# Optimization experiments

Hardware: AMD Instinct MI355X
Metric: run time of the kernel (lower is better)

## Reference

```python
import jax, jax.numpy as jnp
import numpy as np

B, N, D = 2, 2048, 2048
H = 16
HD = D // H  # 128


def setup_inputs() -> dict:
    key = jax.random.key(0)
    k1, k2, k3 = jax.random.split(key, 3)
    x = jax.random.normal(k1, (B, N, D), dtype=jnp.float32)
    # Linear weights stored as [in, out] so y = x @ W matches torch's x @ W.T
    Wq = jax.random.normal(k2, (D, D), dtype=jnp.float32) * (D ** -0.5)
    Wo = jax.random.normal(k3, (D, D), dtype=jnp.float32) * (D ** -0.5)
    bo = jnp.zeros((D,), dtype=jnp.float32)
    return {"x": x, "Wq": Wq, "Wo": Wo, "bo": bo}


def reference(x, Wq, Wo, bo):
    # NOTE: source module (faithfully) projects q, k, v all with q_matrix.
    b, n, d = x.shape
    q = x @ Wq                                   # [B, N, D]
    qh = q.reshape(b, n, H, HD).transpose(0, 2, 1, 3)  # [B, H, N, HD]
    scores = jnp.einsum("bhnd,bhmd->bhnm", qh, qh) * (HD ** -0.5)  # [B,H,N,N]
    attn = jax.nn.softmax(scores, axis=-1)
    y = jnp.einsum("bhnm,bhmd->bhnd", attn, qh)  # [B, H, N, HD]
    y = y.transpose(0, 2, 1, 3).reshape(b, n, d)  # [B, N, D]
    return y @ Wo + bo
```

## Files before the change

kernel.cpp:

```cpp
#include <hip/hip_runtime.h>
#include <hip/hip_bf16.h>

#define BATCH 2
#define SEQ   2048
#define DIM   2048
#define NHEAD 16
#define HDIM  128

#define KSTRIDE 136
#define VSTRIDE 72
#define PSTRIDE 72

typedef __bf16 bf16;
typedef __attribute__((ext_vector_type(2))) __bf16 bf16x2;
typedef __attribute__((ext_vector_type(4))) __bf16 bf16x4;
typedef __attribute__((ext_vector_type(8))) __bf16 bf16x8;
typedef __attribute__((ext_vector_type(4))) float f32x4;

__device__ __forceinline__ void load_lds16(const bf16* g, bf16* l) {
    __builtin_amdgcn_global_load_lds((const __attribute__((address_space(1))) void*)g,
                                     (__attribute__((address_space(3))) void*)l, 16, 0, 0);
}

__device__ __forceinline__ float exp2_hw(float x) { return __builtin_amdgcn_exp2f(x); }

__global__ __launch_bounds__(256)
void prep_kernel(const float* __restrict__ x, bf16* __restrict__ xb,
                 const float* __restrict__ Wq, bf16* __restrict__ Wtq,
                 const float* __restrict__ Wo, bf16* __restrict__ Wto)
{
    __shared__ bf16 T[64 * 72];
    const int bid = blockIdx.x;
    if (bid < 4096) {
        const size_t i = ((size_t)bid * 256 + threadIdx.x) * 8;
        const float4 f0 = *(const float4*)(x + i);
        const float4 f1 = *(const float4*)(x + i + 4);
        *(bf16x8*)(xb + i) = (bf16x8){(bf16)f0.x, (bf16)f0.y, (bf16)f0.z, (bf16)f0.w,
                                      (bf16)f1.x, (bf16)f1.y, (bf16)f1.z, (bf16)f1.w};
        return;
    }
    int t = bid - 4096;
    const float* W  = (t < 1024) ? Wq : Wo;
    bf16*        Wt = (t < 1024) ? Wtq : Wto;
    t &= 1023;
    const int kb = (t >> 5) * 64, nb = (t & 31) * 64;

    const int a = threadIdx.x & 31;
    const int g = threadIdx.x >> 5;
    {
        const float* s0 = W + (size_t)(kb + 2 * a) * DIM + nb + g * 8;
        const float4 r0a = *(const float4*)(s0);
        const float4 r0b = *(const float4*)(s0 + 4);
        const float4 r1a = *(const float4*)(s0 + DIM);
        const float4 r1b = *(const float4*)(s0 + DIM + 4);
        float v0[8] = {r0a.x, r0a.y, r0a.z, r0a.w, r0b.x, r0b.y, r0b.z, r0b.w};
        float v1[8] = {r1a.x, r1a.y, r1a.z, r1a.w, r1b.x, r1b.y, r1b.z, r1b.w};
        #pragma unroll
        for (int i = 0; i < 8; ++i)
            *(bf16x2*)&T[(g * 8 + i) * 72 + 2 * a] = (bf16x2){(bf16)v0[i], (bf16)v1[i]};
    }
    __syncthreads();

    const int r  = threadIdx.x >> 2;
    const int k0 = (threadIdx.x & 3) * 16;
    bf16x8 o0 = *(const bf16x8*)&T[r * 72 + k0];
    bf16x8 o1 = *(const bf16x8*)&T[r * 72 + k0 + 8];
    *(bf16x8*)(Wt + (size_t)(nb + r) * DIM + kb + k0)     = o0;
    *(bf16x8*)(Wt + (size_t)(nb + r) * DIM + kb + k0 + 8) = o1;
}

#define GEMM_PHASE(S, VM, DO_STAGE)                                            \
    {                                                                          \
        const bf16* Aq = Ls + ((S) & 3) * 12288;                               \
        const bf16* Bq = Aq + 4096;                                            \
        bf16x8 a[4], b[4];                                                     \
        _Pragma("unroll")                                                      \
        for (int i = 0; i < 4; ++i) a[i] = *(const bf16x8*)(Aq + offA[i]);     \
        _Pragma("unroll")                                                      \
        for (int j = 0; j < 4; ++j) b[j] = *(const bf16x8*)(Bq + offB[j]);     \
        if (DO_STAGE) {                                                        \
            bf16* lb = Ls + (((S) + 3) & 3) * 12288 + wave * 512;              \
            const int ko = ((S) + 3) * 32;                                     \
            load_lds16(gA + ko, lb);                                           \
            load_lds16(gB0 + ko, lb + 4096);                                   \
            load_lds16(gB1 + ko, lb + 8192);                                   \
        }                                                                      \
        __builtin_amdgcn_s_barrier();                                          \
        __builtin_amdgcn_s_setprio(1);                                         \
        _Pragma("unroll")                                                      \
        for (int i = 0; i < 4; ++i) {                                          \
            _Pragma("unroll")                                                  \
            for (int j = 0; j < 4; ++j)                                        \
                acc[i][j] = __builtin_amdgcn_mfma_f32_16x16x32_bf16(a[i], b[j], acc[i][j], 0, 0, 0); \
        }                                                                      \
        __builtin_amdgcn_s_setprio(0);                                         \
        if ((VM) == 6)      asm volatile("s_waitcnt vmcnt(6)" ::: "memory");   \
        else if ((VM) == 3) asm volatile("s_waitcnt vmcnt(3)" ::: "memory");   \
        else if ((VM) == 0) asm volatile("s_waitcnt vmcnt(0)" ::: "memory");   \
        if ((VM) >= 0) {                                                       \
            __builtin_amdgcn_s_barrier();                                      \
            asm volatile("" ::: "memory");                                     \
        }                                                                      \
    }

template<bool OUT_F32_BIAS>
__global__ __launch_bounds__(512, 2)
void gemm_bt8(const bf16* __restrict__ A, const bf16* __restrict__ Bt,
              const float* __restrict__ bias, void* __restrict__ Cptr,
              int M, int N, int K)
{
    __shared__ bf16 Ls[4 * 12288];

    const int tid  = threadIdx.x;
    const int wave = tid >> 6;
    const int lane = tid & 63;
    const int quad = lane >> 4;
    const int l16  = lane & 15;
    const int wr   = wave >> 2;
    const int wc   = wave & 3;

    const int cpx = gridDim.x >> 3;
    const int logical = (blockIdx.x & 7) * cpx + (blockIdx.x >> 3);
    const int rowBase = (logical >> 3) * 128;
    const int colBase = (logical & 7) * 256;

    int offA[4], offB[4];
    #pragma unroll
    for (int i = 0; i < 4; ++i) {
        int e = (wr * 64 + i * 16 + l16) * 32 + quad * 8;
        offA[i] = e ^ (((e >> 6) & 3) << 3);
    }
    #pragma unroll
    for (int j = 0; j < 4; ++j) {
        int e = (wc * 64 + j * 16 + l16) * 32 + quad * 8;
        offB[j] = e ^ (((e >> 6) & 3) << 3);
    }

    const int oA  = wave * 512 + lane * 8;
    const int eA  = oA ^ (((oA >> 6) & 3) << 3);
    const bf16* gA  = A  + (size_t)(rowBase + (eA >> 5)) * K + (eA & 31);
    const int oB0 = wave * 512 + lane * 8;
    const int eB0 = oB0 ^ (((oB0 >> 6) & 3) << 3);
    const bf16* gB0 = Bt + (size_t)(colBase + (eB0 >> 5)) * K + (eB0 & 31);
    const int oB1 = 4096 + wave * 512 + lane * 8;
    const int eB1 = oB1 ^ (((oB1 >> 6) & 3) << 3);
    const bf16* gB1 = Bt + (size_t)(colBase + ((eB1 - 4096) >> 5) + 128) * K + (eB1 & 31);

    f32x4 acc[4][4] = {};

    #pragma unroll
    for (int s = 0; s < 3; ++s) {
        bf16* lb = Ls + s * 12288 + wave * 512;
        load_lds16(gA  + s * 32, lb);
        load_lds16(gB0 + s * 32, lb + 4096);
        load_lds16(gB1 + s * 32, lb + 8192);
    }
    asm volatile("s_waitcnt vmcnt(6)" ::: "memory");
    __builtin_amdgcn_s_barrier();
    asm volatile("" ::: "memory");

    for (int s = 0; s < 61; ++s)
        GEMM_PHASE(s, 6, true);
    GEMM_PHASE(61, 3, false);
    GEMM_PHASE(62, 0, false);
    GEMM_PHASE(63, -1, false);

    #pragma unroll
    for (int i = 0; i < 4; ++i) {
        #pragma unroll
        for (int j = 0; j < 4; ++j) {
            #pragma unroll
            for (int r = 0; r < 4; ++r) {
                const int row = rowBase + wr * 64 + i * 16 + quad * 4 + r;
                const int col = colBase + wc * 64 + j * 16 + l16;
                const float v = acc[i][j][r];
                if (OUT_F32_BIAS) ((float*)Cptr)[(size_t)row * N + col] = v + bias[col];
                else              ((bf16*)Cptr)[(size_t)row * N + col] = (bf16)v;
            }
        }
    }
}

__global__ __launch_bounds__(256, 2)
void attn_kernel(const bf16* __restrict__ q, bf16* __restrict__ y)
{
    __shared__ bf16 Ks[64 * KSTRIDE];
    __shared__ bf16 Vt[HDIM * VSTRIDE];
    __shared__ bf16 Ps[128 * PSTRIDE];

    const int tid  = threadIdx.x;
    const int wave = tid >> 6;
    const int lane = tid & 63;
    const int quad = lane >> 4;
    const int l16  = lane & 15;

    const int p   = blockIdx.x;
    const int xcd = p & 7;
    const int pos = p >> 3;
    const int g   = xcd * 4 + (pos & 3);
    const int qt  = pos >> 2;
    const int h   = g & 15;
    const int bb  = g >> 4;

    const bf16* qb = q + (size_t)bb * SEQ * DIM + (size_t)h * HDIM;

    const float qs = 0.12752820031096662f;
    bf16x8 aq[2][4];
    #pragma unroll
    for (int nt = 0; nt < 2; ++nt) {
        #pragma unroll
        for (int ks = 0; ks < 4; ++ks) {
            const bf16* src = qb + (size_t)(qt * 128 + wave * 32 + nt * 16 + l16) * DIM + ks * 32 + quad * 8;
            bf16x8 v = *(const bf16x8*)src;
            bf16x8 o;
            #pragma unroll
            for (int e = 0; e < 8; ++e) o[e] = (bf16)((float)v[e] * qs);
            aq[nt][ks] = o;
        }
    }

    float lpart[2] = {0.f, 0.f};
    f32x4 yacc[2][8] = {};

    const int kr   = tid >> 2;
    const int koff = (tid & 3) * 32;
    const int sp   = tid & 31;
    const int ss   = tid >> 5;

    const bf16* srcK = qb + (size_t)kr * DIM + koff;
    const bf16* srcV = qb + (size_t)(2 * sp) * DIM + ss * 16;

    bf16x8 kreg[4], va[2], vb[2];
    #pragma unroll
    for (int c = 0; c < 4; ++c) kreg[c] = *(const bf16x8*)(srcK + c * 8);
    va[0] = *(const bf16x8*)(srcV + 0);
    va[1] = *(const bf16x8*)(srcV + 8);
    vb[0] = *(const bf16x8*)(srcV + DIM + 0);
    vb[1] = *(const bf16x8*)(srcV + DIM + 8);

    for (int kt = 0; kt < SEQ / 64; ++kt) {
        __syncthreads();

        #pragma unroll
        for (int c = 0; c < 4; ++c)
            *(bf16x8*)&Ks[kr * KSTRIDE + koff + c * 8] = kreg[c];
        #pragma unroll
        for (int c = 0; c < 2; ++c)
            #pragma unroll
            for (int e = 0; e < 8; ++e)
                *(bf16x2*)&Vt[(ss * 16 + c * 8 + e) * VSTRIDE + 2 * sp] = (bf16x2){va[c][e], vb[c][e]};

        if (kt + 1 < SEQ / 64) {
            const bf16* nK = srcK + (size_t)(kt + 1) * 64 * DIM;
            const bf16* nV = srcV + (size_t)(kt + 1) * 64 * DIM;
            #pragma unroll
            for (int c = 0; c < 4; ++c) kreg[c] = *(const bf16x8*)(nK + c * 8);
            va[0] = *(const bf16x8*)(nV + 0);
            va[1] = *(const bf16x8*)(nV + 8);
            vb[0] = *(const bf16x8*)(nV + DIM + 0);
            vb[1] = *(const bf16x8*)(nV + DIM + 8);
        }
        __syncthreads();

        #pragma unroll
        for (int mt = 0; mt < 4; ++mt) {
            bf16x8 ak[4];
            #pragma unroll
            for (int ks = 0; ks < 4; ++ks)
                ak[ks] = *(const bf16x8*)&Ks[(mt * 16 + l16) * KSTRIDE + ks * 32 + quad * 8];
            f32x4 s[2] = {};
            __builtin_amdgcn_s_setprio(1);
            #pragma unroll
            for (int ks = 0; ks < 4; ++ks)
                #pragma unroll
                for (int nt = 0; nt < 2; ++nt)
                    s[nt] = __builtin_amdgcn_mfma_f32_16x16x32_bf16(ak[ks], aq[nt][ks], s[nt], 0, 0, 0);
            __builtin_amdgcn_s_setprio(0);
            #pragma unroll
            for (int nt = 0; nt < 2; ++nt) {
                float p0 = exp2_hw(s[nt][0]);
                float p1 = exp2_hw(s[nt][1]);
                float p2 = exp2_hw(s[nt][2]);
                float p3 = exp2_hw(s[nt][3]);
                lpart[nt] += (p0 + p1) + (p2 + p3);
                *(bf16x4*)&Ps[(wave * 32 + nt * 16 + l16) * PSTRIDE + mt * 16 + quad * 4] =
                    (bf16x4){(bf16)p0, (bf16)p1, (bf16)p2, (bf16)p3};
            }
        }

        #pragma unroll
        for (int ks2 = 0; ks2 < 2; ++ks2) {
            bf16x8 ap[2];
            #pragma unroll
            for (int i = 0; i < 2; ++i)
                ap[i] = *(const bf16x8*)&Ps[(wave * 32 + i * 16 + l16) * PSTRIDE + ks2 * 32 + quad * 8];
            __builtin_amdgcn_s_setprio(1);
            #pragma unroll
            for (int n = 0; n < 8; ++n) {
                bf16x8 bv = *(const bf16x8*)&Vt[(n * 16 + l16) * VSTRIDE + ks2 * 32 + quad * 8];
                #pragma unroll
                for (int i = 0; i < 2; ++i)
                    yacc[i][n] = __builtin_amdgcn_mfma_f32_16x16x32_bf16(ap[i], bv, yacc[i][n], 0, 0, 0);
            }
            __builtin_amdgcn_s_setprio(0);
        }
    }

    float lfull[2];
    #pragma unroll
    for (int nt = 0; nt < 2; ++nt) {
        float l = lpart[nt];
        l += __shfl_xor(l, 16);
        l += __shfl_xor(l, 32);
        lfull[nt] = l;
    }

    bf16* yb = y + (size_t)bb * SEQ * DIM + (size_t)(qt * 128) * DIM + (size_t)h * HDIM;
    #pragma unroll
    for (int i = 0; i < 2; ++i) {
        #pragma unroll
        for (int r = 0; r < 4; ++r) {
            const float lv  = __shfl(lfull[i], (lane & 48) | (quad * 4 + r));
            const float inv = 1.f / lv;
            const int row = wave * 32 + i * 16 + quad * 4 + r;
            #pragma unroll
            for (int n = 0; n < 8; ++n)
                yb[(size_t)row * DIM + n * 16 + l16] = (bf16)(yacc[i][n][r] * inv);
        }
    }
}

extern "C" void kernel_launch(void* const* d_in, const int* in_sizes, int n_in,
                              void* d_out, int out_size, void* d_ws, size_t ws_size,
                              hipStream_t stream)
{
    const float* x  = (const float*)d_in[0];
    const float* Wq = (const float*)d_in[1];
    const float* Wo = (const float*)d_in[2];
    const float* bo = (const float*)d_in[3];
    float* out = (float*)d_out;

    const size_t NELEM = (size_t)BATCH * SEQ * DIM;
    bf16* qws = (bf16*)d_ws;
    bf16* yws = qws + NELEM;
    bf16* Wtq = yws;
    bf16* Wto = qws + 2 * NELEM;
    bf16* xb  = (bf16*)d_out;

    const int M = BATCH * SEQ;

    prep_kernel<<<6144, 256, 0, stream>>>(x, xb, Wq, Wtq, Wo, Wto);
    gemm_bt8<false><<<256, 512, 0, stream>>>(xb, Wtq, nullptr, qws, M, DIM, DIM);
    attn_kernel<<<512, 256, 0, stream>>>(qws, yws);
    gemm_bt8<true><<<256, 512, 0, stream>>>(yws, Wto, bo, out, M, DIM, DIM);
}
```

Measured before the change: 264.8 us.

## Stream K tiles via direct global-to-LDS loads into XOR-swizzled double buffer

K tiles now go straight from global memory into LDS with global_load_lds, skipping the register staging, into a double buffer that is filled one tile ahead. A padded row stride is replaced by an XOR swizzle on the column to avoid bank conflicts. All 16 K fragments for the tile are read from LDS before the MFMA loop starts. This adds LDS use (two unpadded 64x128 buffers) and more live registers, which may hurt occupancy at two blocks per CU. It also depends on the async LDS writes being visible after the barrier.

```diff
diff --git a/kernel.cpp b/kernel.cpp
--- a/kernel.cpp
+++ b/kernel.cpp
@@ -7,7 +7,6 @@
 #define NHEAD 16
 #define HDIM  128
 
-#define KSTRIDE 136
 #define VSTRIDE 72
 #define PSTRIDE 72
 
@@ -184,7 +183,7 @@
 __global__ __launch_bounds__(256, 2)
 void attn_kernel(const bf16* __restrict__ q, bf16* __restrict__ y)
 {
-    __shared__ bf16 Ks[64 * KSTRIDE];
+    __shared__ bf16 Ks[2 * 64 * 128];
     __shared__ bf16 Vt[HDIM * VSTRIDE];
     __shared__ bf16 Ps[128 * PSTRIDE];
 
@@ -222,17 +221,17 @@
     float lpart[2] = {0.f, 0.f};
     f32x4 yacc[2][8] = {};
 
-    const int kr   = tid >> 2;
-    const int koff = (tid & 3) * 32;
+    const int colK = ((((tid & 15) << 4) ^ (((tid >> 4) & 7) << 4)) >> 1);
+    const bf16* srcK = qb + (size_t)(tid >> 4) * DIM + colK;
+
     const int sp   = tid & 31;
     const int ss   = tid >> 5;
-
-    const bf16* srcK = qb + (size_t)kr * DIM + koff;
     const bf16* srcV = qb + (size_t)(2 * sp) * DIM + ss * 16;
 
-    bf16x8 kreg[4], va[2], vb[2];
-    #pragma unroll
-    for (int c = 0; c < 4; ++c) kreg[c] = *(const bf16x8*)(srcK + c * 8);
+    #pragma unroll
+    for (int c = 0; c < 4; ++c)
+        load_lds16(srcK + (size_t)c * 16 * DIM, Ks + tid * 8 + c * 2048);
+    bf16x8 va[2], vb[2];
     va[0] = *(const bf16x8*)(srcV + 0);
     va[1] = *(const bf16x8*)(srcV + 8);
     vb[0] = *(const bf16x8*)(srcV + DIM + 0);
@@ -241,9 +240,14 @@
     for (int kt = 0; kt < SEQ / 64; ++kt) {
         __syncthreads();
 
-        #pragma unroll
-        for (int c = 0; c < 4; ++c)
-            *(bf16x8*)&Ks[kr * KSTRIDE + koff + c * 8] = kreg[c];
+        if (kt + 1 < SEQ / 64) {
+            bf16* kd = Ks + ((kt + 1) & 1) * 8192 + tid * 8;
+            const bf16* kg = srcK + (size_t)(kt + 1) * 64 * DIM;
+            #pragma unroll
+            for (int c = 0; c < 4; ++c)
+                load_lds16(kg + (size_t)c * 16 * DIM, kd + c * 2048);
+        }
+
         #pragma unroll
         for (int c = 0; c < 2; ++c)
             #pragma unroll
@@ -251,30 +255,35 @@
                 *(bf16x2*)&Vt[(ss * 16 + c * 8 + e) * VSTRIDE + 2 * sp] = (bf16x2){va[c][e], vb[c][e]};
 
         if (kt + 1 < SEQ / 64) {
-            const bf16* nK = srcK + (size_t)(kt + 1) * 64 * DIM;
             const bf16* nV = srcV + (size_t)(kt + 1) * 64 * DIM;
-            #pragma unroll
-            for (int c = 0; c < 4; ++c) kreg[c] = *(const bf16x8*)(nK + c * 8);
             va[0] = *(const bf16x8*)(nV + 0);
             va[1] = *(const bf16x8*)(nV + 8);
             vb[0] = *(const bf16x8*)(nV + DIM + 0);
             vb[1] = *(const bf16x8*)(nV + DIM + 8);
         }
         __syncthreads();
-
+        asm volatile("" ::: "memory");
+
+        const bf16* Kb = Ks + (kt & 1) * 8192;
+        bf16x8 akr[4][4];
         #pragma unroll
         for (int mt = 0; mt < 4; ++mt) {
-            bf16x8 ak[4];
-            #pragma unroll
-            for (int ks = 0; ks < 4; ++ks)
-                ak[ks] = *(const bf16x8*)&Ks[(mt * 16 + l16) * KSTRIDE + ks * 32 + quad * 8];
+            #pragma unroll
+            for (int ks = 0; ks < 4; ++ks) {
+                const int cb = (ks * 64 + quad * 16) ^ ((l16 & 7) << 4);
+                akr[mt][ks] = *(const bf16x8*)(Kb + (mt * 16 + l16) * 128 + (cb >> 1));
+            }
+        }
+
+        #pragma unroll
+        for (int mt = 0; mt < 4; ++mt) {
             f32x4 s[2] = {};
             __builtin_amdgcn_s_setprio(1);
             #pragma unroll
             for (int ks = 0; ks < 4; ++ks)
                 #pragma unroll
                 for (int nt = 0; nt < 2; ++nt)
-                    s[nt] = __builtin_amdgcn_mfma_f32_16x16x32_bf16(ak[ks], aq[nt][ks], s[nt], 0, 0, 0);
+                    s[nt] = __builtin_amdgcn_mfma_f32_16x16x32_bf16(akr[mt][ks], aq[nt][ks], s[nt], 0, 0, 0);
             __builtin_amdgcn_s_setprio(0);
             #pragma unroll
             for (int nt = 0; nt < 2; ++nt) {
```

Result: slower. 273.9 us (+3.4%).
